# Kernel optimization log

Measured on AMD Instinct MI355X. Metric: run time of the kernel, lower is better.

The kernel has to match this reference:

```python
import jax, jax.numpy as jnp
import numpy as np

B, T, D, H, C, S = 1024, 64, 512, 512, 96, 21  # batch, enc_len, input_size, hidden, num_classes, decode steps


def setup_inputs() -> dict:
    key = jax.random.key(0)
    ks = jax.random.split(key, 12)
    sc = lambda n: 1.0 / np.sqrt(n)
    return {
        "batch_H": jax.random.normal(ks[0], (B, T, D), jnp.float32),
        "text": jax.random.randint(ks[1], (B, S), 0, C),
        "Wi": jax.random.normal(ks[2], (H, D), jnp.float32) * sc(D),
        "Wh": jax.random.normal(ks[3], (H, H), jnp.float32) * sc(H),
        "bh": jax.random.normal(ks[4], (H,), jnp.float32) * sc(H),
        "Ws": jax.random.normal(ks[5], (1, H), jnp.float32) * sc(H),
        "Wih": jax.random.normal(ks[6], (4 * H, D + C), jnp.float32) * sc(H),
        "Whh": jax.random.normal(ks[7], (4 * H, H), jnp.float32) * sc(H),
        "bih": jax.random.normal(ks[8], (4 * H,), jnp.float32) * sc(H),
        "bhh": jax.random.normal(ks[9], (4 * H,), jnp.float32) * sc(H),
        "Wg": jax.random.normal(ks[10], (C, H), jnp.float32) * sc(H),
        "bg": jax.random.normal(ks[11], (C,), jnp.float32) * sc(H),
    }


def reference(batch_H, text, Wi, Wh, bh, Ws, Wih, Whh, bih, bhh, Wg, bg):
    # Teacher-forced (is_train=True) path; dropout is identity (eval mode / p=0).
    # Precompute i2h(batch_H) once -- the per-step result is identical.
    Hp = jnp.einsum('btd,hd->bth', batch_H, Wi)  # [B,T,H]
    onehots = jax.nn.one_hot(text, C, dtype=batch_H.dtype)  # [B,S,C]

    def step(carry, oh):
        h, c = carry
        ph = h @ Wh.T + bh                              # h2h(prev_hidden[0])  [B,H]
        e = jnp.tanh(Hp + ph[:, None, :]) @ Ws[0]       # score -> [B,T]
        alpha = jax.nn.softmax(e, axis=1)               # softmax over enc steps
        ctx = jnp.einsum('bt,btd->bd', alpha, batch_H)  # bmm context  [B,D]
        x = jnp.concatenate([ctx, oh], axis=1)          # [B, D+C]
        gates = x @ Wih.T + bih + h @ Whh.T + bhh       # LSTMCell gates [B,4H]
        i_g, f_g, g_g, o_g = jnp.split(gates, 4, axis=1)  # torch gate order i,f,g,o
        c2 = jax.nn.sigmoid(f_g) * c + jax.nn.sigmoid(i_g) * jnp.tanh(g_g)
        h2 = jax.nn.sigmoid(o_g) * jnp.tanh(c2)
        return (h2, c2), h2

    init = (jnp.zeros((B, H), batch_H.dtype), jnp.zeros((B, H), batch_H.dtype))
    _, hs = jax.lax.scan(step, init, jnp.swapaxes(onehots, 0, 1))  # hs: [S,B,H]
    output_hiddens = jnp.swapaxes(hs, 0, 1)                        # [B,S,H]
    probs = output_hiddens @ Wg.T + bg                             # generator [B,S,C]
    return probs
```

## Files before the change

### kernel.cpp

```cpp
#include <hip/hip_runtime.h>
#include <hip/hip_bf16.h>
#include <math.h>

using bf16 = __hip_bfloat16;

#define NB 1024
#define NT 64
#define ND 512
#define NH 512
#define NC 96
#define NS 21
#define NDC 608
#define NG 2048
#define NWC 2688

#define OFF_HPB   0u
#define OFF_BHB   16777216u
#define OFF_C     33554432u
#define OFF_HB16  34078720u
#define OFF_PH    34340864u
#define OFF_CTXB  34865152u
#define OFF_GATES 35127296u
#define OFF_WIB   37224448u
#define OFF_WHCG  37355520u
#define OFF_WIHB  38043648u
#define OFF_BIHH  38567936u
#define OFF_BH_   38569984u
#define OFF_WS_   38570496u
#define OFF_BG_   38571008u
#define OFF_OH    38571104u
#define WS_NEED_FLOATS 38767712u
#define WS_NEED_BYTES ((size_t)WS_NEED_FLOATS * 4u)

typedef __attribute__((ext_vector_type(8))) short bf16x8;
typedef __attribute__((ext_vector_type(4))) float f32x4;

__device__ __forceinline__ unsigned short f2bu(float f) {
    unsigned u = __float_as_uint(f);
    unsigned r = (u + 0x7fffu + ((u >> 16) & 1u)) >> 16;
    return (unsigned short)r;
}
__device__ __forceinline__ float b2f(short s) {
    return __uint_as_float(((unsigned)(unsigned short)s) << 16);
}
__device__ __forceinline__ float fast_sigmoid(float x) {
    return 1.f / (1.f + __expf(-x));
}
__device__ __forceinline__ float fast_tanh(float x) {
    x = fminf(15.f, fmaxf(-15.f, x));
    float e = __expf(2.f * x);
    return (e - 1.f) / (e + 1.f);
}

#define BH_BLOCKS 32768u
#define W_ELEMS   2886752u
#define W_BLOCKS  ((W_ELEMS + 255u) / 256u)

__global__ __launch_bounds__(256) void conv_all(
    const float* __restrict__ bHsrc,
    const float* __restrict__ Wi, const float* __restrict__ Wh, const float* __restrict__ bh,
    const float* __restrict__ Ws, const float* __restrict__ Wih, const float* __restrict__ Whh,
    const float* __restrict__ bih, const float* __restrict__ bhh, const float* __restrict__ Wg,
    const float* __restrict__ bg, float* __restrict__ ws) {
    if (blockIdx.x < BH_BLOCKS) {
        unsigned short* dst = (unsigned short*)(ws + OFF_BHB);
        size_t i = ((size_t)blockIdx.x * 256 + threadIdx.x) * 4;
        float4 v = *(const float4*)(bHsrc + i);
        uint2 pk;
        pk.x = (unsigned)f2bu(v.x) | ((unsigned)f2bu(v.y) << 16);
        pk.y = (unsigned)f2bu(v.z) | ((unsigned)f2bu(v.w) << 16);
        *(uint2*)&dst[i] = pk;
        return;
    }
    unsigned i = (blockIdx.x - BH_BLOCKS) * 256u + threadIdx.x;
    if (i >= W_ELEMS) return;
    unsigned short* WiB  = (unsigned short*)(ws + OFF_WIB);
    unsigned short* WcB  = (unsigned short*)(ws + OFF_WHCG);
    unsigned short* WihB = (unsigned short*)(ws + OFF_WIHB);
    if (i < 262144u) {
        WiB[i] = f2bu(Wi[i]);
    } else if (i < 524288u) {
        unsigned j = i - 262144u;
        WcB[j] = f2bu(Wh[j]);
    } else if (i < 1572864u) {
        unsigned j = i - 524288u;
        WcB[262144u + j] = f2bu(Whh[j]);
    } else if (i < 1622016u) {
        unsigned j = i - 1572864u;
        WcB[1310720u + j] = f2bu(Wg[j]);
    } else if (i < 1638400u) {
        unsigned j = i - 1622016u;
        WcB[1359872u + j] = 0;
    } else if (i < 2686976u) {
        unsigned j = i - 1638400u;
        unsigned row = j >> 9, col = j & 511u;
        WihB[j] = f2bu(Wih[row * NDC + col]);
    } else if (i < 2689024u) {
        unsigned j = i - 2686976u;
        ws[OFF_BIHH + j] = bih[j] + bhh[j];
    } else if (i < 2689536u) {
        unsigned j = i - 2689024u;
        ws[OFF_BH_ + j] = bh[j];
    } else if (i < 2690048u) {
        unsigned j = i - 2689536u;
        ws[OFF_WS_ + j] = Ws[j];
    } else if (i < 2690144u) {
        unsigned j = i - 2690048u;
        ws[OFF_BG_ + j] = bg[j];
    } else {
        unsigned j = i - 2690144u;
        unsigned c = j >> 11, n = j & 2047u;
        ws[OFF_OH + j] = Wih[(size_t)n * NDC + ND + c];
    }
}

__global__ __launch_bounds__(256) void hp_gemm(const bf16* __restrict__ A,
                                               const bf16* __restrict__ B,
                                               bf16* __restrict__ outB) {
    __shared__ short As[128 * 40];
    __shared__ short Bs[128 * 40];
    const int tid = threadIdx.x;
    const int wave = tid >> 6, lane = tid & 63;
    const int wrow = wave >> 1, wcol = wave & 1;
    const int quad = lane >> 4, l16 = lane & 15;
    const int m0 = blockIdx.x * 128, n0 = blockIdx.y * 128;
    f32x4 acc[4][4];
    #pragma unroll
    for (int mi = 0; mi < 4; ++mi)
        #pragma unroll
        for (int ni = 0; ni < 4; ++ni) acc[mi][ni] = (f32x4){0.f, 0.f, 0.f, 0.f};
    for (int k0 = 0; k0 < 512; k0 += 32) {
        #pragma unroll
        for (int l = 0; l < 2; ++l) {
            int c = tid + l * 256;
            int row = c >> 2, c8 = c & 3;
            *(uint4*)&As[row * 40 + c8 * 8] =
                *(const uint4*)&A[(size_t)(m0 + row) * 512 + k0 + c8 * 8];
            *(uint4*)&Bs[row * 40 + c8 * 8] =
                *(const uint4*)&B[(size_t)(n0 + row) * 512 + k0 + c8 * 8];
        }
        __syncthreads();
        bf16x8 af[4], bfr[4];
        #pragma unroll
        for (int mi = 0; mi < 4; ++mi)
            af[mi] = *(const bf16x8*)&As[(wrow * 64 + mi * 16 + l16) * 40 + quad * 8];
        #pragma unroll
        for (int ni = 0; ni < 4; ++ni)
            bfr[ni] = *(const bf16x8*)&Bs[(wcol * 64 + ni * 16 + l16) * 40 + quad * 8];
        #pragma unroll
        for (int mi = 0; mi < 4; ++mi)
            #pragma unroll
            for (int ni = 0; ni < 4; ++ni)
                acc[mi][ni] = __builtin_amdgcn_mfma_f32_16x16x32_bf16(af[mi], bfr[ni],
                                                                      acc[mi][ni], 0, 0, 0);
        __syncthreads();
    }
    #pragma unroll
    for (int mi = 0; mi < 4; ++mi)
        #pragma unroll
        for (int ni = 0; ni < 4; ++ni)
            #pragma unroll
            for (int r = 0; r < 4; ++r) {
                int m = m0 + wrow * 64 + mi * 16 + quad * 4 + r;
                int n = n0 + wcol * 64 + ni * 16 + l16;
                outB[(size_t)m * 512 + n] = __float2bfloat16(acc[mi][ni][r]);
            }
}

__global__ __launch_bounds__(256) void combo_gemm(const bf16* __restrict__ A,
                                                  const bf16* __restrict__ B,
                                                  const float* __restrict__ bh,
                                                  const float* __restrict__ bihh,
                                                  const float* __restrict__ bg,
                                                  unsigned short* __restrict__ phB,
                                                  float* __restrict__ gates,
                                                  float* __restrict__ out, int s) {
    __shared__ short As[128 * 40];
    __shared__ short Bs[64 * 40];
    const int tid = threadIdx.x;
    const int wave = tid >> 6, lane = tid & 63;
    const int wrow = wave >> 1, wcol = wave & 1;
    const int quad = lane >> 4, l16 = lane & 15;
    const int m0 = blockIdx.x * 128, n0 = blockIdx.y * 64;
    f32x4 acc[4][2];
    #pragma unroll
    for (int mi = 0; mi < 4; ++mi)
        #pragma unroll
        for (int ni = 0; ni < 2; ++ni) acc[mi][ni] = (f32x4){0.f, 0.f, 0.f, 0.f};
    for (int k0 = 0; k0 < 512; k0 += 32) {
        #pragma unroll
        for (int l = 0; l < 2; ++l) {
            int c = tid + l * 256;
            int row = c >> 2, c8 = c & 3;
            *(uint4*)&As[row * 40 + c8 * 8] =
                *(const uint4*)&A[(size_t)(m0 + row) * 512 + k0 + c8 * 8];
        }
        {
            int row = tid >> 2, c8 = tid & 3;
            *(uint4*)&Bs[row * 40 + c8 * 8] =
                *(const uint4*)&B[(size_t)(n0 + row) * 512 + k0 + c8 * 8];
        }
        __syncthreads();
        bf16x8 af[4], bfr[2];
        #pragma unroll
        for (int mi = 0; mi < 4; ++mi)
            af[mi] = *(const bf16x8*)&As[(wrow * 64 + mi * 16 + l16) * 40 + quad * 8];
        #pragma unroll
        for (int ni = 0; ni < 2; ++ni)
            bfr[ni] = *(const bf16x8*)&Bs[(wcol * 32 + ni * 16 + l16) * 40 + quad * 8];
        #pragma unroll
        for (int mi = 0; mi < 4; ++mi)
            #pragma unroll
            for (int ni = 0; ni < 2; ++ni)
                acc[mi][ni] = __builtin_amdgcn_mfma_f32_16x16x32_bf16(af[mi], bfr[ni],
                                                                      acc[mi][ni], 0, 0, 0);
        __syncthreads();
    }
    #pragma unroll
    for (int mi = 0; mi < 4; ++mi) {
        #pragma unroll
        for (int ni = 0; ni < 2; ++ni) {
            #pragma unroll
            for (int r = 0; r < 4; ++r) {
                int m = m0 + wrow * 64 + mi * 16 + quad * 4 + r;
                int n = n0 + wcol * 32 + ni * 16 + l16;
                float v = acc[mi][ni][r];
                if (n < NH) {
                    phB[(size_t)m * NH + n] = f2bu(v + bh[n]);
                } else if (n < NH + NG) {
                    gates[(size_t)m * NG + (n - NH)] = v + bihh[n - NH];
                } else if (n < NH + NG + NC) {
                    if (s > 0)
                        out[(size_t)m * (NS * NC) + (s - 1) * NC + (n - NH - NG)] =
                            v + bg[n - NH - NG];
                }
            }
        }
    }
}

__global__ __launch_bounds__(256, 4) void attn_fused(const bf16* __restrict__ Hp,
                                                     const bf16* __restrict__ phB,
                                                     const float* __restrict__ Wsv,
                                                     const bf16* __restrict__ bH,
                                                     unsigned short* __restrict__ ctxB) {
    const int b = blockIdx.x;
    const int tid = threadIdx.x;
    const int wave = tid >> 6, lane = tid & 63;
    __shared__ float tr[64 * 65];
    __shared__ float salpha[NT];
    __shared__ float red[4][520];
    bf16x8 phv = *(const bf16x8*)(phB + (size_t)b * NH + lane * 8);
    float4 wsa = *(const float4*)(Wsv + lane * 8);
    float4 wsb = *(const float4*)(Wsv + lane * 8 + 4);
    float ph8[8], ws8[8];
    #pragma unroll
    for (int j = 0; j < 8; ++j) ph8[j] = b2f(phv[j]);
    ws8[0] = wsa.x; ws8[1] = wsa.y; ws8[2] = wsa.z; ws8[3] = wsa.w;
    ws8[4] = wsb.x; ws8[5] = wsb.y; ws8[6] = wsb.z; ws8[7] = wsb.w;
    const bf16* hpb = Hp + ((size_t)b * NT + wave * 16) * NH + lane * 8;
    float acc[16];
    #pragma unroll
    for (int i = 0; i < 16; ++i) {
        bf16x8 hv = *(const bf16x8*)(hpb + (size_t)i * NH);
        float s = 0.f;
        #pragma unroll
        for (int j = 0; j < 8; ++j) s += fast_tanh(b2f(hv[j]) + ph8[j]) * ws8[j];
        acc[i] = s;
    }
    #pragma unroll
    for (int i = 0; i < 16; ++i) tr[(wave * 16 + i) * 65 + lane] = acc[i];
    __syncthreads();
    if (tid < NT) {
        const float* row = &tr[tid * 65];
        float e = 0.f;
        #pragma unroll
        for (int j = 0; j < 64; ++j) e += row[j];
        float m = e;
        #pragma unroll
        for (int off = 32; off > 0; off >>= 1) m = fmaxf(m, __shfl_xor(m, off, 64));
        float ex = __expf(e - m);
        float ssum = ex;
        #pragma unroll
        for (int off = 32; off > 0; off >>= 1) ssum += __shfl_xor(ssum, off, 64);
        salpha[tid] = ex / ssum;
    }
    __syncthreads();
    {
        const bf16* bh = bH + ((size_t)b * NT + wave * 16) * ND + lane * 8;
        float a8[8];
        #pragma unroll
        for (int u = 0; u < 8; ++u) a8[u] = 0.f;
        #pragma unroll
        for (int i = 0; i < 16; ++i) {
            float al = salpha[wave * 16 + i];
            bf16x8 v = *(const bf16x8*)(bh + (size_t)i * ND);
            #pragma unroll
            for (int u = 0; u < 8; ++u) a8[u] = fmaf(al, b2f(v[u]), a8[u]);
        }
        #pragma unroll
        for (int u = 0; u < 8; ++u) red[wave][lane * 8 + u] = a8[u];
    }
    __syncthreads();
    for (int d = tid; d < ND; d += 256) {
        float sum = red[0][d] + red[1][d] + red[2][d] + red[3][d];
        ctxB[(size_t)b * ND + d] = f2bu(sum);
    }
}

__global__ __launch_bounds__(256) void gates_lstm(const bf16* __restrict__ ctxB,
                                                  const bf16* __restrict__ WihB,
                                                  const float* __restrict__ gates_pre,
                                                  const float* __restrict__ onehotT,
                                                  const int* __restrict__ text, int s,
                                                  float* __restrict__ c,
                                                  unsigned short* __restrict__ hB) {
    __shared__ float smem[4 * 32 * 65];
    short* As = (short*)smem;
    short* Bs = As + 32 * 40;
    float* ex = smem;
    const int tid = threadIdx.x;
    const int g = tid >> 6, lane = tid & 63;
    const int quad = lane >> 4, l16 = lane & 15;
    const int m0 = blockIdx.x * 32, kp0 = blockIdx.y * 64;
    f32x4 acc[2][4];
    #pragma unroll
    for (int mi = 0; mi < 2; ++mi)
        #pragma unroll
        for (int ni = 0; ni < 4; ++ni) acc[mi][ni] = (f32x4){0.f, 0.f, 0.f, 0.f};
    for (int k0 = 0; k0 < 512; k0 += 32) {
        if (tid < 128) {
            int row = tid >> 2, c8 = tid & 3;
            *(uint4*)&As[row * 40 + c8 * 8] =
                *(const uint4*)&ctxB[(size_t)(m0 + row) * 512 + k0 + c8 * 8];
        }
        #pragma unroll
        for (int l = 0; l < 4; ++l) {
            int j = tid + l * 256;
            int row = j >> 2, c8 = j & 3;
            int brow = (row >> 6) * 512 + kp0 + (row & 63);
            *(uint4*)&Bs[row * 40 + c8 * 8] =
                *(const uint4*)&WihB[(size_t)brow * 512 + k0 + c8 * 8];
        }
        __syncthreads();
        bf16x8 af[2], bfr[4];
        #pragma unroll
        for (int mi = 0; mi < 2; ++mi)
            af[mi] = *(const bf16x8*)&As[(mi * 16 + l16) * 40 + quad * 8];
        #pragma unroll
        for (int ni = 0; ni < 4; ++ni)
            bfr[ni] = *(const bf16x8*)&Bs[(g * 64 + ni * 16 + l16) * 40 + quad * 8];
        #pragma unroll
        for (int mi = 0; mi < 2; ++mi)
            #pragma unroll
            for (int ni = 0; ni < 4; ++ni)
                acc[mi][ni] = __builtin_amdgcn_mfma_f32_16x16x32_bf16(af[mi], bfr[ni],
                                                                      acc[mi][ni], 0, 0, 0);
        __syncthreads();
    }
    #pragma unroll
    for (int mi = 0; mi < 2; ++mi)
        #pragma unroll
        for (int ni = 0; ni < 4; ++ni)
            #pragma unroll
            for (int r = 0; r < 4; ++r) {
                int ml = mi * 16 + quad * 4 + r;
                int nl = ni * 16 + l16;
                ex[g * 2080 + ml * 65 + nl] = acc[mi][ni][r];
            }
    __syncthreads();
    #pragma unroll 1
    for (int t = 0; t < 8; ++t) {
        int idx = tid + t * 256;
        int ml = idx >> 6, kl = idx & 63;
        int m = m0 + ml, kp = kp0 + kl;
        int tb = text[m * NS + s];
        const float* oh = onehotT + (size_t)tb * NG;
        const float* gp = gates_pre + (size_t)m * NG;
        float ig = fast_sigmoid(ex[0 * 2080 + ml * 65 + kl] + gp[kp] + oh[kp]);
        float fg = fast_sigmoid(ex[1 * 2080 + ml * 65 + kl] + gp[NH + kp] + oh[NH + kp]);
        float gg = fast_tanh(ex[2 * 2080 + ml * 65 + kl] + gp[2 * NH + kp] + oh[2 * NH + kp]);
        float og = fast_sigmoid(ex[3 * 2080 + ml * 65 + kl] + gp[3 * NH + kp] + oh[3 * NH + kp]);
        float cn = fg * c[(size_t)m * NH + kp] + ig * gg;
        float hn = og * fast_tanh(cn);
        c[(size_t)m * NH + kp] = cn;
        hB[(size_t)m * NH + kp] = f2bu(hn);
    }
}

__global__ __launch_bounds__(256) void final_gen(const bf16* __restrict__ hB,
                                                 const bf16* __restrict__ WgB,
                                                 const float* __restrict__ bg,
                                                 float* __restrict__ out) {
    const int b = blockIdx.x;
    const int tid = threadIdx.x;
    __shared__ float hsm[NH];
    for (int k = tid; k < NH; k += 256) hsm[k] = b2f(*(const short*)&hB[(size_t)b * NH + k]);
    __syncthreads();
    if (tid < 2 * NC) {
        int oc = tid >> 1, half = tid & 1;
        const bf16* w = WgB + (size_t)oc * NH + half * 256;
        float a = 0.f;
        #pragma unroll 4
        for (int j = 0; j < 32; ++j) {
            bf16x8 w8 = *(const bf16x8*)(w + j * 8);
            #pragma unroll
            for (int u = 0; u < 8; ++u)
                a = fmaf(b2f(w8[u]), hsm[half * 256 + j * 8 + u], a);
        }
        a += __shfl_xor(a, 1, 64);
        if (half == 0)
            out[(size_t)b * (NS * NC) + 20 * NC + oc] = a + bg[oc];
    }
}

extern "C" void kernel_launch(void* const* d_in, const int* in_sizes, int n_in,
                              void* d_out, int out_size, void* d_ws, size_t ws_size,
                              hipStream_t stream) {
    if (ws_size < WS_NEED_BYTES) {
        hipMemsetAsync(d_out, 0x7F, (size_t)out_size * 4, stream);
        return;
    }
    float* ws = (float*)d_ws;
    bf16* HpB  = (bf16*)(ws + OFF_HPB);
    bf16* bHB  = (bf16*)(ws + OFF_BHB);
    float* cb  = ws + OFF_C;
    bf16* hB   = (bf16*)(ws + OFF_HB16);
    bf16* phB  = (bf16*)(ws + OFF_PH);
    bf16* ctxB = (bf16*)(ws + OFF_CTXB);
    float* gb  = ws + OFF_GATES;
    bf16* WiB  = (bf16*)(ws + OFF_WIB);
    bf16* WcB  = (bf16*)(ws + OFF_WHCG);
    bf16* WihB = (bf16*)(ws + OFF_WIHB);
    const int* text = (const int*)d_in[1];
    float* out = (float*)d_out;

    conv_all<<<BH_BLOCKS + W_BLOCKS, 256, 0, stream>>>(
        (const float*)d_in[0],
        (const float*)d_in[2], (const float*)d_in[3], (const float*)d_in[4],
        (const float*)d_in[5], (const float*)d_in[6], (const float*)d_in[7],
        (const float*)d_in[8], (const float*)d_in[9], (const float*)d_in[10],
        (const float*)d_in[11], ws);
    hipMemsetAsync(cb, 0, (size_t)786432 * 4, stream);

    hp_gemm<<<dim3(NB * NT / 128, ND / 128), 256, 0, stream>>>(bHB, WiB, HpB);

    for (int s = 0; s < NS; ++s) {
        combo_gemm<<<dim3(NB / 128, NWC / 64), 256, 0, stream>>>(
            hB, WcB, ws + OFF_BH_, ws + OFF_BIHH, ws + OFF_BG_,
            (unsigned short*)phB, gb, out, s);
        attn_fused<<<NB, 256, 0, stream>>>(HpB, phB, ws + OFF_WS_, bHB,
                                           (unsigned short*)ctxB);
        gates_lstm<<<dim3(NB / 32, NH / 64), 256, 0, stream>>>(
            ctxB, WihB, gb, ws + OFF_OH, text, s, cb, (unsigned short*)hB);
    }
    final_gen<<<NB, 256, 0, stream>>>(hB, WcB + (size_t)2560 * 512, ws + OFF_BG_, out);
}
```

Before: 1.690 ms.

## Fuse Whh recurrent GEMM into LSTM gate kernel with concatenated K and ping-pong h

The h@Whh term moves out of combo_gemm and into gates_lstm, which now runs K=1024 over [ctx|h] against a concatenated bf16 Wih|Whh matrix. The fp32 gates_pre buffer write and read are dropped, and the biases are folded into the one-hot table. Two h buffers are ping-ponged so the old h stays readable while the new one is written. Sigmoid and tanh now use the hardware reciprocal without clamping, and the attention row reduction is split across four waves. The cost is a longer serial K loop in gates_lstm, which runs only 256 blocks.

```diff
diff --git a/kernel.cpp b/kernel.cpp
--- a/kernel.cpp
+++ b/kernel.cpp
@@ -12,7 +12,7 @@
 #define NS 21
 #define NDC 608
 #define NG 2048
-#define NWC 2688
+#define NWC2 640
 
 #define OFF_HPB   0u
 #define OFF_BHB   16777216u
@@ -20,11 +20,10 @@
 #define OFF_HB16  34078720u
 #define OFF_PH    34340864u
 #define OFF_CTXB  34865152u
-#define OFF_GATES 35127296u
+#define OFF_WCB   35127296u
+#define OFF_WIH2  35291136u
+#define OFF_HB2   36339712u
 #define OFF_WIB   37224448u
-#define OFF_WHCG  37355520u
-#define OFF_WIHB  38043648u
-#define OFF_BIHH  38567936u
 #define OFF_BH_   38569984u
 #define OFF_WS_   38570496u
 #define OFF_BG_   38571008u
@@ -44,16 +43,14 @@
     return __uint_as_float(((unsigned)(unsigned short)s) << 16);
 }
 __device__ __forceinline__ float fast_sigmoid(float x) {
-    return 1.f / (1.f + __expf(-x));
+    return __builtin_amdgcn_rcpf(1.f + __expf(-x));
 }
 __device__ __forceinline__ float fast_tanh(float x) {
-    x = fminf(15.f, fmaxf(-15.f, x));
-    float e = __expf(2.f * x);
-    return (e - 1.f) / (e + 1.f);
+    return 1.f - 2.f * __builtin_amdgcn_rcpf(1.f + __expf(2.f * x));
 }
 
 #define BH_BLOCKS 32768u
-#define W_ELEMS   2886752u
+#define W_ELEMS   2884704u
 #define W_BLOCKS  ((W_ELEMS + 255u) / 256u)
 
 __global__ __launch_bounds__(256) void conv_all(
@@ -75,42 +72,40 @@
     unsigned i = (blockIdx.x - BH_BLOCKS) * 256u + threadIdx.x;
     if (i >= W_ELEMS) return;
     unsigned short* WiB  = (unsigned short*)(ws + OFF_WIB);
-    unsigned short* WcB  = (unsigned short*)(ws + OFF_WHCG);
-    unsigned short* WihB = (unsigned short*)(ws + OFF_WIHB);
+    unsigned short* WcB  = (unsigned short*)(ws + OFF_WCB);
+    unsigned short* Wih2 = (unsigned short*)(ws + OFF_WIH2);
     if (i < 262144u) {
         WiB[i] = f2bu(Wi[i]);
     } else if (i < 524288u) {
         unsigned j = i - 262144u;
         WcB[j] = f2bu(Wh[j]);
-    } else if (i < 1572864u) {
+    } else if (i < 573440u) {
         unsigned j = i - 524288u;
-        WcB[262144u + j] = f2bu(Whh[j]);
-    } else if (i < 1622016u) {
-        unsigned j = i - 1572864u;
-        WcB[1310720u + j] = f2bu(Wg[j]);
+        WcB[262144u + j] = f2bu(Wg[j]);
+    } else if (i < 589824u) {
+        unsigned j = i - 573440u;
+        WcB[311296u + j] = 0;
     } else if (i < 1638400u) {
-        unsigned j = i - 1622016u;
-        WcB[1359872u + j] = 0;
+        unsigned j = i - 589824u;
+        unsigned row = j >> 9, col = j & 511u;
+        Wih2[row * 1024u + col] = f2bu(Wih[(size_t)row * NDC + col]);
     } else if (i < 2686976u) {
         unsigned j = i - 1638400u;
         unsigned row = j >> 9, col = j & 511u;
-        WihB[j] = f2bu(Wih[row * NDC + col]);
-    } else if (i < 2689024u) {
+        Wih2[row * 1024u + 512u + col] = f2bu(Whh[j]);
+    } else if (i < 2687488u) {
         unsigned j = i - 2686976u;
-        ws[OFF_BIHH + j] = bih[j] + bhh[j];
-    } else if (i < 2689536u) {
-        unsigned j = i - 2689024u;
         ws[OFF_BH_ + j] = bh[j];
-    } else if (i < 2690048u) {
-        unsigned j = i - 2689536u;
+    } else if (i < 2688000u) {
+        unsigned j = i - 2687488u;
         ws[OFF_WS_ + j] = Ws[j];
-    } else if (i < 2690144u) {
-        unsigned j = i - 2690048u;
+    } else if (i < 2688096u) {
+        unsigned j = i - 2688000u;
         ws[OFF_BG_ + j] = bg[j];
     } else {
-        unsigned j = i - 2690144u;
+        unsigned j = i - 2688096u;
         unsigned c = j >> 11, n = j & 2047u;
-        ws[OFF_OH + j] = Wih[(size_t)n * NDC + ND + c];
+        ws[OFF_OH + j] = Wih[(size_t)n * NDC + ND + c] + bih[n] + bhh[n];
     }
 }
 
@@ -170,10 +165,8 @@
 __global__ __launch_bounds__(256) void combo_gemm(const bf16* __restrict__ A,
                                                   const bf16* __restrict__ B,
                                                   const float* __restrict__ bh,
-                                                  const float* __restrict__ bihh,
                                                   const float* __restrict__ bg,
                                                   unsigned short* __restrict__ phB,
-                                                  float* __restrict__ gates,
                                                   float* __restrict__ out, int s) {
     __shared__ short As[128 * 40];
     __shared__ short Bs[64 * 40];
@@ -227,12 +220,9 @@
                 float v = acc[mi][ni][r];
                 if (n < NH) {
                     phB[(size_t)m * NH + n] = f2bu(v + bh[n]);
-                } else if (n < NH + NG) {
-                    gates[(size_t)m * NG + (n - NH)] = v + bihh[n - NH];
-                } else if (n < NH + NG + NC) {
+                } else if (n < NH + NC) {
                     if (s > 0)
-                        out[(size_t)m * (NS * NC) + (s - 1) * NC + (n - NH - NG)] =
-                            v + bg[n - NH - NG];
+                        out[(size_t)m * (NS * NC) + (s - 1) * NC + (n - NH)] = v + bg[n - NH];
                 }
             }
         }
@@ -259,23 +249,26 @@
     ws8[0] = wsa.x; ws8[1] = wsa.y; ws8[2] = wsa.z; ws8[3] = wsa.w;
     ws8[4] = wsb.x; ws8[5] = wsb.y; ws8[6] = wsb.z; ws8[7] = wsb.w;
     const bf16* hpb = Hp + ((size_t)b * NT + wave * 16) * NH + lane * 8;
-    float acc[16];
     #pragma unroll
     for (int i = 0; i < 16; ++i) {
         bf16x8 hv = *(const bf16x8*)(hpb + (size_t)i * NH);
         float s = 0.f;
         #pragma unroll
         for (int j = 0; j < 8; ++j) s += fast_tanh(b2f(hv[j]) + ph8[j]) * ws8[j];
-        acc[i] = s;
-    }
-    #pragma unroll
-    for (int i = 0; i < 16; ++i) tr[(wave * 16 + i) * 65 + lane] = acc[i];
+        tr[(wave * 16 + i) * 65 + lane] = s;
+    }
+    __syncthreads();
+    {
+        int t = tid & 63, ch = tid >> 6;
+        const float* row = &tr[t * 65 + ch * 16];
+        float p = 0.f;
+        #pragma unroll
+        for (int j = 0; j < 16; ++j) p += row[j];
+        red[ch][t] = p;
+    }
     __syncthreads();
     if (tid < NT) {
-        const float* row = &tr[tid * 65];
-        float e = 0.f;
-        #pragma unroll
-        for (int j = 0; j < 64; ++j) e += row[j];
+        float e = red[0][tid] + red[1][tid] + red[2][tid] + red[3][tid];
         float m = e;
         #pragma unroll
         for (int off = 32; off > 0; off >>= 1) m = fmaxf(m, __shfl_xor(m, off, 64));
@@ -309,12 +302,12 @@
 }
 
 __global__ __launch_bounds__(256) void gates_lstm(const bf16* __restrict__ ctxB,
-                                                  const bf16* __restrict__ WihB,
-                                                  const float* __restrict__ gates_pre,
-                                                  const float* __restrict__ onehotT,
+                                                  const bf16* __restrict__ hIn,
+                                                  const bf16* __restrict__ Wih2,
+                                                  const float* __restrict__ ohb,
                                                   const int* __restrict__ text, int s,
                                                   float* __restrict__ c,
-                                                  unsigned short* __restrict__ hB) {
+                                                  unsigned short* __restrict__ hOut) {
     __shared__ float smem[4 * 32 * 65];
     short* As = (short*)smem;
     short* Bs = As + 32 * 40;
@@ -328,11 +321,13 @@
     for (int mi = 0; mi < 2; ++mi)
         #pragma unroll
         for (int ni = 0; ni < 4; ++ni) acc[mi][ni] = (f32x4){0.f, 0.f, 0.f, 0.f};
-    for (int k0 = 0; k0 < 512; k0 += 32) {
+    for (int k0 = 0; k0 < 1024; k0 += 32) {
         if (tid < 128) {
             int row = tid >> 2, c8 = tid & 3;
-            *(uint4*)&As[row * 40 + c8 * 8] =
-                *(const uint4*)&ctxB[(size_t)(m0 + row) * 512 + k0 + c8 * 8];
+            const bf16* src = (k0 < 512)
+                ? ctxB + (size_t)(m0 + row) * 512 + k0 + c8 * 8
+                : hIn + (size_t)(m0 + row) * 512 + (k0 - 512) + c8 * 8;
+            *(uint4*)&As[row * 40 + c8 * 8] = *(const uint4*)src;
         }
         #pragma unroll
         for (int l = 0; l < 4; ++l) {
@@ -340,7 +335,7 @@
             int row = j >> 2, c8 = j & 3;
             int brow = (row >> 6) * 512 + kp0 + (row & 63);
             *(uint4*)&Bs[row * 40 + c8 * 8] =
-                *(const uint4*)&WihB[(size_t)brow * 512 + k0 + c8 * 8];
+                *(const uint4*)&Wih2[(size_t)brow * 1024 + k0 + c8 * 8];
         }
         __syncthreads();
         bf16x8 af[2], bfr[4];
@@ -375,16 +370,15 @@
         int ml = idx >> 6, kl = idx & 63;
         int m = m0 + ml, kp = kp0 + kl;
         int tb = text[m * NS + s];
-        const float* oh = onehotT + (size_t)tb * NG;
-        const float* gp = gates_pre + (size_t)m * NG;
-        float ig = fast_sigmoid(ex[0 * 2080 + ml * 65 + kl] + gp[kp] + oh[kp]);
-        float fg = fast_sigmoid(ex[1 * 2080 + ml * 65 + kl] + gp[NH + kp] + oh[NH + kp]);
-        float gg = fast_tanh(ex[2 * 2080 + ml * 65 + kl] + gp[2 * NH + kp] + oh[2 * NH + kp]);
-        float og = fast_sigmoid(ex[3 * 2080 + ml * 65 + kl] + gp[3 * NH + kp] + oh[3 * NH + kp]);
+        const float* oh = ohb + (size_t)tb * NG;
+        float ig = fast_sigmoid(ex[0 * 2080 + ml * 65 + kl] + oh[kp]);
+        float fg = fast_sigmoid(ex[1 * 2080 + ml * 65 + kl] + oh[NH + kp]);
+        float gg = fast_tanh(ex[2 * 2080 + ml * 65 + kl] + oh[2 * NH + kp]);
+        float og = fast_sigmoid(ex[3 * 2080 + ml * 65 + kl] + oh[3 * NH + kp]);
         float cn = fg * c[(size_t)m * NH + kp] + ig * gg;
         float hn = og * fast_tanh(cn);
         c[(size_t)m * NH + kp] = cn;
-        hB[(size_t)m * NH + kp] = f2bu(hn);
+        hOut[(size_t)m * NH + kp] = f2bu(hn);
     }
 }
 
@@ -425,13 +419,13 @@
     bf16* HpB  = (bf16*)(ws + OFF_HPB);
     bf16* bHB  = (bf16*)(ws + OFF_BHB);
     float* cb  = ws + OFF_C;
-    bf16* hB   = (bf16*)(ws + OFF_HB16);
+    bf16* h0   = (bf16*)(ws + OFF_HB16);
+    bf16* h1   = (bf16*)(ws + OFF_HB2);
     bf16* phB  = (bf16*)(ws + OFF_PH);
     bf16* ctxB = (bf16*)(ws + OFF_CTXB);
-    float* gb  = ws + OFF_GATES;
+    bf16* WcB  = (bf16*)(ws + OFF_WCB);
+    bf16* Wih2 = (bf16*)(ws + OFF_WIH2);
     bf16* WiB  = (bf16*)(ws + OFF_WIB);
-    bf16* WcB  = (bf16*)(ws + OFF_WHCG);
-    bf16* WihB = (bf16*)(ws + OFF_WIHB);
     const int* text = (const int*)d_in[1];
     float* out = (float*)d_out;
 
@@ -446,13 +440,14 @@
     hp_gemm<<<dim3(NB * NT / 128, ND / 128), 256, 0, stream>>>(bHB, WiB, HpB);
 
     for (int s = 0; s < NS; ++s) {
-        combo_gemm<<<dim3(NB / 128, NWC / 64), 256, 0, stream>>>(
-            hB, WcB, ws + OFF_BH_, ws + OFF_BIHH, ws + OFF_BG_,
-            (unsigned short*)phB, gb, out, s);
+        bf16* hcur = (s & 1) ? h1 : h0;
+        bf16* hnext = (s & 1) ? h0 : h1;
+        combo_gemm<<<dim3(NB / 128, NWC2 / 64), 256, 0, stream>>>(
+            hcur, WcB, ws + OFF_BH_, ws + OFF_BG_, (unsigned short*)phB, out, s);
         attn_fused<<<NB, 256, 0, stream>>>(HpB, phB, ws + OFF_WS_, bHB,
                                            (unsigned short*)ctxB);
         gates_lstm<<<dim3(NB / 32, NH / 64), 256, 0, stream>>>(
-            ctxB, WihB, gb, ws + OFF_OH, text, s, cb, (unsigned short*)hB);
-    }
-    final_gen<<<NB, 256, 0, stream>>>(hB, WcB + (size_t)2560 * 512, ws + OFF_BG_, out);
-}
+            ctxB, hcur, Wih2, ws + OFF_OH, text, s, cb, (unsigned short*)hnext);
+    }
+    final_gen<<<NB, 256, 0, stream>>>(h1, WcB + (size_t)512 * 512, ws + OFF_BG_, out);
+}
```

After: 1.664 ms. No clear change (-1.5%).
